# Performance work log

Hardware: AMD Instinct MI355X
Metric: run time of the kernel (lower is better)

## Reference

```python
import jax, jax.numpy as jnp
import numpy as np
from math import factorial, sqrt

L_OUT = 4      # max_degree / max_actp_degree -> 25 sph components
L_B = 2        # max_basis_degree -> 9 sph components
F = 16         # num_radial_features (feature channels)
N_ATOMS = 10000
N_BONDS = 80000
CUTOFF = 5.0

# ---------------- real Clebsch-Gordan coefficients (numpy, at import) ----------

def _cg(j1, m1, j2, m2, j3, m3):
    if m1 + m2 != m3 or not (abs(j1 - j2) <= j3 <= j1 + j2):
        return 0.0
    f = factorial
    pre = sqrt((2 * j3 + 1) * f(j1 + j2 - j3) * f(j1 - j2 + j3) * f(-j1 + j2 + j3) / f(j1 + j2 + j3 + 1))
    pre *= sqrt(f(j1 + m1) * f(j1 - m1) * f(j2 + m2) * f(j2 - m2) * f(j3 + m3) * f(j3 - m3))
    s = 0.0
    kmin = max(0, j2 - j3 - m1, j1 - j3 + m2)
    kmax = min(j1 + j2 - j3, j1 - m1, j2 + m2)
    for k in range(kmin, kmax + 1):
        s += (-1) ** k / (f(k) * f(j1 + j2 - j3 - k) * f(j1 - m1 - k) * f(j2 + m2 - k) * f(j3 - j2 + m1 + k) * f(j3 - j1 - m2 + k))
    return pre * s

def _U(l):
    # complex->real spherical harmonic change of basis (Condon-Shortley)
    U = np.zeros((2 * l + 1, 2 * l + 1), dtype=complex)
    U[l, l] = 1.0
    for m in range(1, l + 1):
        U[l + m, l + m] = (-1) ** m / np.sqrt(2.0)
        U[l + m, l - m] = 1.0 / np.sqrt(2.0)
        U[l - m, l + m] = -1j * (-1) ** m / np.sqrt(2.0)
        U[l - m, l - m] = 1j / np.sqrt(2.0)
    return U

def _real_cg(l1, l2, l3):
    Cc = np.zeros((2 * l1 + 1, 2 * l2 + 1, 2 * l3 + 1), dtype=complex)
    for m1 in range(-l1, l1 + 1):
        for m2 in range(-l2, l2 + 1):
            m3 = m1 + m2
            if -l3 <= m3 <= l3:
                Cc[l1 + m1, l2 + m2, l3 + m3] = _cg(l1, m1, l2, m2, l3, m3)
    Cr = np.einsum('am,bn,ck,mnk->abc', _U(l1).conj(), _U(l2).conj(), _U(l3), Cc)
    out = Cr.real + Cr.imag  # exactly one of the two is nonzero per path
    out[np.abs(out) < 1e-12] = 0.0
    return out

PATHS = []
for _l1 in range(L_B + 1):
    for _l2 in range(L_OUT + 1):
        for _l3 in range(abs(_l1 - _l2), min(_l1 + _l2, L_OUT) + 1):
            PATHS.append((_l1, _l2, _l3, jnp.asarray(_real_cg(_l1, _l2, _l3), dtype=jnp.float32)))
N_PATHS = len(PATHS)

# ---------------- equivariant building blocks --------------------------------

def _sph(u):
    # real spherical harmonics l=0..2, m=-l..l, for unit vectors u (E,3)
    x, y, z = u[:, 0], u[:, 1], u[:, 2]
    c0 = 0.28209479177387814
    c1 = 0.4886025119029199
    c2a = 1.0925484305920792
    c2b = 0.31539156525252005
    c2c = 0.5462742152960396
    return jnp.stack([jnp.full_like(x, c0),
                      c1 * y, c1 * z, c1 * x,
                      c2a * x * y, c2a * y * z, c2b * (3 * z * z - 1.0), c2a * x * z, c2c * (x * x - y * y)],
                     axis=-1)  # (E,9)

def basis(disp):
    r = jnp.linalg.norm(disp, axis=-1)
    u = disp / (r[:, None] + 1e-12)
    Y = _sph(u)  # (E,9)
    centers = jnp.linspace(0.0, CUTOFF, F)
    width = CUTOFF / F
    rb = jnp.exp(-((r[:, None] - centers) / width) ** 2)  # (E,F)
    cut = jnp.where(r < CUTOFF, 0.5 * (jnp.cos(jnp.pi * r / CUTOFF) + 1.0), 0.0)
    rb = rb * cut[:, None]
    return Y[:, None, :, None] * rb[:, None, None, :]

def edense(x, W, b):
    # per-(parity,degree) feature mixing; bias only on even scalar channel
    nl = W.shape[1]
    outs = []
    for l in range(nl):
        lo, hi = l * l, (l + 1) * (l + 1)
        outs.append(jnp.einsum('epmf,pfg->epmg', x[:, :, lo:hi], W[:, l]))
    out = jnp.concatenate(outs, axis=2)
    return out.at[:, 0, 0, :].add(b)

def eln(x, gamma, beta, eps=1e-5):
    # equivariant LayerNorm: RMS of per-feature degree norms; standard LN on even scalar
    outs = []
    for l in range(L_OUT + 1):
        lo, hi = l * l, (l + 1) * (l + 1)
        blk = x[:, :, lo:hi]
        n2 = jnp.sum(blk * blk, axis=2)                       # (E,2,F)
        rms = jnp.sqrt(jnp.mean(n2, axis=-1, keepdims=True) + eps)  # (E,2,1)
        outs.append(blk / rms[..., None] * gamma[:, l][None, :, None, :])
    out = jnp.concatenate(outs, axis=2)
    s = x[:, 0, 0, :]
    mu = jnp.mean(s, axis=-1, keepdims=True)
    var = jnp.var(s, axis=-1, keepdims=True)
    sh = (s - mu) / jnp.sqrt(var + eps) * gamma[0, 0] + beta
    return out.at[:, 0, 0, :].set(sh)

def emish(x):
    s = x[:, 0, 0, :]
    sp = jax.nn.softplus(s)
    t = jnp.tanh(sp)
    f = s * t
    fp = t + s * (1.0 - t * t) * jax.nn.sigmoid(s)
    out = x * fp[:, None, None, :]
    return out.at[:, 0, 0, :].set(f)

def tensor_product(x1, x2, Wtp):
    # FusedTensor analogue: x1 (E,1,9,F) parity (-1)^l per degree; x2 (E,2,25,F)
    x1s = x1[:, 0]
    out = jnp.zeros_like(x2)
    for i, (l1, l2, l3, C) in enumerate(PATHS):
        a = x1s[:, l1 * l1:(l1 + 1) * (l1 + 1)]          # (E,n1,F)
        b = x2[:, :, l2 * l2:(l2 + 1) * (l2 + 1)]        # (E,2,n2,F)
        tmp = jnp.einsum('enf,epmf,nmk->epkf', a, b, C)  # (E,2,n3,F)
        tmp = tmp * Wtp[i][None, :, None, :]
        if l1 % 2 == 1:
            tmp = tmp[:, ::-1]  # odd l1 flips output parity
        out = out.at[:, :, l3 * l3:(l3 + 1) * (l3 + 1)].add(tmp)
    return out

def forward(atomic_descriptors, neighbour_indices, neighbour_displacements,
            W1, b1, gamma, beta, W2, b2, Wb, bb, Wtp):
    i, j = neighbour_indices[:, 0], neighbour_indices[:, 1]
    y = atomic_descriptors[i] + atomic_descriptors[j]  # (E,2,25,F)
    y = edense(y, W1, b1)
    y = eln(y, gamma, beta)
    y = emish(y)
    y = edense(y, W2, b2) + y
    be = basis(neighbour_displacements).astype(jnp.float32)  # (E,1,9,F)
    bed = edense(be, Wb, bb)
    return tensor_product(bed, y, Wtp)

# ---------------- harness ----------------------------------------------------

def setup_inputs() -> dict:
    key = jax.random.key(0)
    ks = jax.random.split(key, 8)
    scale = 1.0 / np.sqrt(F)
    return {
        'atomic_descriptors': jax.random.normal(ks[0], (N_ATOMS, 2, (L_OUT + 1) ** 2, F), jnp.float32),
        'neighbour_indices': jax.random.randint(ks[1], (N_BONDS, 2), 0, N_ATOMS),
        'neighbour_displacements': jax.random.normal(ks[2], (N_BONDS, 3), jnp.float32),
        'W1': jax.random.normal(ks[3], (2, L_OUT + 1, F, F), jnp.float32) * scale,
        'b1': jnp.zeros((F,), jnp.float32),
        'gamma': jnp.ones((2, L_OUT + 1, F), jnp.float32),
        'beta': jnp.zeros((F,), jnp.float32),
        'W2': jax.random.normal(ks[4], (2, L_OUT + 1, F, F), jnp.float32) * scale,
        'b2': jnp.zeros((F,), jnp.float32),
        'Wb': jax.random.normal(ks[5], (1, L_B + 1, F, F), jnp.float32) * scale,
        'bb': jnp.zeros((F,), jnp.float32),
        'Wtp': jax.random.normal(ks[6], (N_PATHS, 2, F), jnp.float32) * scale,
    }

def reference(atomic_descriptors, neighbour_indices, neighbour_displacements,
              W1, b1, gamma, beta, W2, b2, Wb, bb, Wtp):
    return forward(atomic_descriptors, neighbour_indices, neighbour_displacements,
                   W1, b1, gamma, beta, W2, b2, Wb, bb, Wtp)
```

## Files before the change

### kernel.cpp

```cpp
#include <hip/hip_runtime.h>
#include <hip/hip_fp16.h>

#define NF   16
#define NLM  25
#define BPB  16
#define YSTR 816

typedef _Float16 h2f __attribute__((ext_vector_type(2)));

#if defined(__has_builtin)
#if __has_builtin(__builtin_amdgcn_fdot2)
#define FDOT2(a,b,c) __builtin_amdgcn_fdot2((a),(b),(c),false)
#endif
#endif
#ifndef FDOT2
#define FDOT2(a,b,c) ((c) + (float)(a)[0]*(float)(b)[0] + (float)(a)[1]*(float)(b)[1])
#endif

#define WAVE_LDS_FENCE() asm volatile("" ::: "memory")

#define NT_STORE(p, v) __builtin_nontemporal_store((v), (p))

constexpr double FT[12] = {1.,1.,2.,6.,24.,120.,720.,5040.,40320.,362880.,3628800.,39916800.};

constexpr double csqrt(double x){
    if (x <= 0.0) return 0.0;
    double g = x > 1.0 ? x : 1.0;
    for (int i = 0; i < 60; ++i){ double n = 0.5*(g + x/g); if (n == g) break; g = n; }
    return g;
}

constexpr double cgc(int j1,int m1,int j2,int m2,int j3,int m3){
    if (m1 + m2 != m3) return 0.0;
    int dj = j1 > j2 ? j1 - j2 : j2 - j1;
    if (j3 < dj || j3 > j1 + j2) return 0.0;
    if (m1 < -j1 || m1 > j1 || m2 < -j2 || m2 > j2 || m3 < -j3 || m3 > j3) return 0.0;
    double X = (2*j3+1)*FT[j1+j2-j3]*FT[j1-j2+j3]*FT[-j1+j2+j3]/FT[j1+j2+j3+1];
    double Y = FT[j1+m1]*FT[j1-m1]*FT[j2+m2]*FT[j2-m2]*FT[j3+m3]*FT[j3-m3];
    double pre = csqrt(X*Y);
    double s = 0.0;
    int kmin = 0; if (j2-j3-m1 > kmin) kmin = j2-j3-m1; if (j1-j3+m2 > kmin) kmin = j1-j3+m2;
    int kmax = j1+j2-j3; if (j1-m1 < kmax) kmax = j1-m1; if (j2+m2 < kmax) kmax = j2+m2;
    for (int k = kmin; k <= kmax; ++k)
        s += ((k & 1) ? -1.0 : 1.0) /
             (FT[k]*FT[j1+j2-j3-k]*FT[j1-m1-k]*FT[j2+m2-k]*FT[j3-j2+m1+k]*FT[j3-j1-m2+k]);
    return pre*s;
}

struct cplx { double re, im; };

constexpr cplx Uent(int l, int a, int col){
    int mp = a - l, mm = col - l;
    const double s2 = 0.70710678118654752440;
    if (mp == 0) return (mm == 0) ? cplx{1.0,0.0} : cplx{0.0,0.0};
    if (mp > 0){
        double sgn = (mp & 1) ? -1.0 : 1.0;
        if (mm ==  mp) return cplx{sgn*s2, 0.0};
        if (mm == -mp) return cplx{s2, 0.0};
        return cplx{0.0,0.0};
    }
    int q = -mp; double sgn = (q & 1) ? -1.0 : 1.0;
    if (mm ==  q) return cplx{0.0, -sgn*s2};
    if (mm == -q) return cplx{0.0,  s2};
    return cplx{0.0,0.0};
}

constexpr double realcg(int l1,int l2,int l3,int a,int b,int c){
    double re = 0.0, im = 0.0;
    for (int m = -l1; m <= l1; ++m){
        cplx u1 = Uent(l1, a, l1+m); u1.im = -u1.im;
        if (u1.re == 0.0 && u1.im == 0.0) continue;
        for (int n = -l2; n <= l2; ++n){
            cplx u2 = Uent(l2, b, l2+n); u2.im = -u2.im;
            if (u2.re == 0.0 && u2.im == 0.0) continue;
            int k = m + n; if (k < -l3 || k > l3) continue;
            cplx u3 = Uent(l3, c, l3+k);
            if (u3.re == 0.0 && u3.im == 0.0) continue;
            double g = cgc(l1, m, l2, n, l3, k);
            if (g == 0.0) continue;
            double pr = u1.re*u2.re - u1.im*u2.im;
            double pi = u1.re*u2.im + u1.im*u2.re;
            re += (pr*u3.re - pi*u3.im)*g;
            im += (pr*u3.im + pi*u3.re)*g;
        }
    }
    double o = re + im;
    if (o < 1e-12 && o > -1e-12) o = 0.0;
    return o;
}

template<int L1,int L2,int L3> struct CGT { float v[2*L1+1][2*L2+1][2*L3+1]; };

template<int L1,int L2,int L3>
constexpr CGT<L1,L2,L3> makeCG(){
    CGT<L1,L2,L3> t{};
    for (int a = 0; a < 2*L1+1; ++a)
        for (int b = 0; b < 2*L2+1; ++b)
            for (int c = 0; c < 2*L3+1; ++c)
                t.v[a][b][c] = (float)realcg(L1, L2, L3, a, b, c);
    return t;
}

template<int L1,int L2,int L3,int PIDX>
__device__ __forceinline__ void tp_path(const float (&bed)[9], const float (&y)[2][NLM],
                                        float (&o)[2][NLM], const float* __restrict__ Wtp, int g){
    static constexpr CGT<L1,L2,L3> C = makeCG<L1,L2,L3>();
    constexpr int K = 2*L3+1;
    float a0[K], a1[K];
    #pragma unroll
    for (int k = 0; k < K; ++k){ a0[k] = 0.f; a1[k] = 0.f; }
    #pragma unroll
    for (int n = 0; n < 2*L1+1; ++n){
        const float bn = bed[L1*L1 + n];
        #pragma unroll
        for (int m = 0; m < 2*L2+1; ++m){
            const float p0 = bn * y[0][L2*L2 + m];
            const float p1 = bn * y[1][L2*L2 + m];
            #pragma unroll
            for (int k = 0; k < K; ++k){
                const float c = C.v[n][m][k];
                if (c != 0.f){
                    a0[k] = fmaf(c, p0, a0[k]);
                    a1[k] = fmaf(c, p1, a1[k]);
                }
            }
        }
    }
    const float w0 = Wtp[(PIDX*2 + 0)*NF + g];
    const float w1 = Wtp[(PIDX*2 + 1)*NF + g];
    #pragma unroll
    for (int k = 0; k < K; ++k){
        if (L1 & 1){
            o[0][L3*L3 + k] = fmaf(w1, a1[k], o[0][L3*L3 + k]);
            o[1][L3*L3 + k] = fmaf(w0, a0[k], o[1][L3*L3 + k]);
        } else {
            o[0][L3*L3 + k] = fmaf(w0, a0[k], o[0][L3*L3 + k]);
            o[1][L3*L3 + k] = fmaf(w1, a1[k], o[1][L3*L3 + k]);
        }
    }
}

__global__ void transpose_w(const float* __restrict__ W1, const float* __restrict__ W2,
                            const float* __restrict__ Wb, void* __restrict__ wsv){
    __half* h1 = (__half*)wsv;
    __half* h2 = h1 + 2560;
    float*  wb = (float*)(h1 + 5120);
    int idx = blockIdx.x*256 + threadIdx.x;
    if (idx < 2560){
        int mat = idx >> 8, r = (idx >> 4) & 15, c = idx & 15;
        h1[idx] = __float2half_rn(W1[mat*256 + c*16 + r]);
        h2[idx] = __float2half_rn(W2[mat*256 + c*16 + r]);
    } else if (idx < 3328){
        int k = idx - 2560; int mat = k >> 8, r = (k >> 4) & 15, c = k & 15;
        wb[k] = Wb[mat*256 + c*16 + r];
    }
}

struct H8 { float4 a, b; };

__global__ __launch_bounds__(256, 3)
void bctmd_kernel(const float* __restrict__ A, const int* __restrict__ nbr,
                  const float* __restrict__ disp,
                  const float* __restrict__ b1, const float* __restrict__ gamma,
                  const float* __restrict__ beta, const float* __restrict__ b2,
                  const float* __restrict__ bb, const float* __restrict__ Wtp,
                  const __half* __restrict__ Wt1h, const __half* __restrict__ Wt2h,
                  const float* __restrict__ Wtb,
                  float* __restrict__ out, int nb)
{
    __shared__ __align__(16) __half ybuf[BPB*YSTR];
    const int tid  = threadIdx.x;
    const int bl   = tid >> 4;
    const int g    = tid & 15;
    const int bond = blockIdx.x*BPB + bl;
    const bool act = bond < nb;
    __half* yb = &ybuf[bl*YSTR];

    if (act){
        const int i = nbr[2*bond], j = nbr[2*bond+1];
        const float4* Ai = (const float4*)(A + (size_t)i*800);
        const float4* Aj = (const float4*)(A + (size_t)j*800);
        #pragma unroll
        for (int it = 0; it < 13; ++it){
            int q = g + 16*it;
            if (q < 200){
                float4 a = Ai[q], b = Aj[q];
                __half2* d = (__half2*)&yb[4*q];
                d[0] = __float22half2_rn(make_float2(a.x+b.x, a.y+b.y));
                d[1] = __float22half2_rn(make_float2(a.z+b.z, a.w+b.w));
            }
        }
    }
    WAVE_LDS_FENCE();

    float y[2][NLM];
    if (act){
        #pragma unroll
        for (int p = 0; p < 2; ++p){
            #pragma unroll
            for (int l = 0; l < 5; ++l){
                H8 wv = *(const H8*)(Wt1h + (((p*5 + l)*16 + g) << 4));
                const h2f* w = (const h2f*)&wv;
                #pragma unroll
                for (int m = 0; m < 2*l+1; ++m){
                    const int lm = l*l + m;
                    H8 rv = *(const H8*)&yb[p*400 + lm*16];
                    const h2f* v = (const h2f*)&rv;
                    float acc = 0.f;
                    #pragma unroll
                    for (int q = 0; q < 8; ++q) acc = FDOT2(v[q], w[q], acc);
                    y[p][lm] = acc;
                }
            }
        }
        y[0][0] += b1[g];

        float s0 = y[0][0];
        #pragma unroll
        for (int p = 0; p < 2; ++p){
            #pragma unroll
            for (int l = 0; l < 5; ++l){
                float n2 = 0.f;
                #pragma unroll
                for (int m = 0; m < 2*l+1; ++m){ float v = y[p][l*l+m]; n2 = fmaf(v, v, n2); }
                #pragma unroll
                for (int d = 1; d < 16; d <<= 1) n2 += __shfl_xor(n2, d, 16);
                float rinv = rsqrtf(n2*(1.f/16.f) + 1e-5f);
                float sc = rinv * gamma[(p*5 + l)*16 + g];
                #pragma unroll
                for (int m = 0; m < 2*l+1; ++m) y[p][l*l+m] *= sc;
            }
        }
        float mu = s0, sq = s0*s0;
        #pragma unroll
        for (int d = 1; d < 16; d <<= 1){ mu += __shfl_xor(mu, d, 16); sq += __shfl_xor(sq, d, 16); }
        mu *= (1.f/16.f); sq *= (1.f/16.f);
        float var = sq - mu*mu;
        float sh = (s0 - mu)*rsqrtf(var + 1e-5f)*gamma[g] + beta[g];
        y[0][0] = sh;

        float s  = sh;
        float es = __expf(fminf(s, 30.f));
        float es2 = es*es;
        float t   = (es2 + 2.f*es) / (es2 + 2.f*es + 2.f);
        float sig = es / (1.f + es);
        float fv  = s*t;
        float fp  = t + s*(1.f - t*t)*sig;
        #pragma unroll
        for (int p = 0; p < 2; ++p)
            #pragma unroll
            for (int lm = 0; lm < NLM; ++lm) y[p][lm] *= fp;
        y[0][0] = fv;
    }
    WAVE_LDS_FENCE();

    if (act){
        #pragma unroll
        for (int p = 0; p < 2; ++p)
            #pragma unroll
            for (int lm = 0; lm < NLM; ++lm)
                yb[p*400 + lm*16 + g] = __float2half_rn(y[p][lm]);
    }
    WAVE_LDS_FENCE();

    if (act){
        #pragma unroll
        for (int p = 0; p < 2; ++p){
            #pragma unroll
            for (int l = 0; l < 5; ++l){
                H8 wv = *(const H8*)(Wt2h + (((p*5 + l)*16 + g) << 4));
                const h2f* w = (const h2f*)&wv;
                #pragma unroll
                for (int m = 0; m < 2*l+1; ++m){
                    const int lm = l*l + m;
                    H8 rv = *(const H8*)&yb[p*400 + lm*16];
                    const h2f* v = (const h2f*)&rv;
                    float acc = 0.f;
                    #pragma unroll
                    for (int q = 0; q < 8; ++q) acc = FDOT2(v[q], w[q], acc);
                    y[p][lm] += acc;
                }
            }
        }
        y[0][0] += b2[g];

        float dx = disp[3*bond], dy = disp[3*bond+1], dz = disp[3*bond+2];
        float r  = sqrtf(dx*dx + dy*dy + dz*dz);
        float ir = 1.f/(r + 1e-12f);
        float ux = dx*ir, uy = dy*ir, uz = dz*ir;
        float Y[9];
        Y[0] = 0.28209479177387814f;
        Y[1] = 0.4886025119029199f*uy; Y[2] = 0.4886025119029199f*uz; Y[3] = 0.4886025119029199f*ux;
        Y[4] = 1.0925484305920792f*ux*uy; Y[5] = 1.0925484305920792f*uy*uz;
        Y[6] = 0.31539156525252005f*(3.f*uz*uz - 1.f);
        Y[7] = 1.0925484305920792f*ux*uz; Y[8] = 0.5462742152960396f*(ux*ux - uy*uy);
        float cut = (r < 5.0f) ? 0.5f*(__cosf(r*0.62831853071795864769f) + 1.f) : 0.f;
        float rb[16];
        #pragma unroll
        for (int f = 0; f < 16; ++f){
            float d = (r - (float)f*(1.f/3.f))*3.2f;
            rb[f] = __expf(-d*d)*cut;
        }
        float t3[3];
        #pragma unroll
        for (int l = 0; l < 3; ++l){
            const float4* wp = (const float4*)(Wtb + (l*16 + g)*16);
            float acc = 0.f;
            #pragma unroll
            for (int q = 0; q < 4; ++q){
                float4 t = wp[q];
                acc = fmaf(rb[4*q],   t.x, acc);
                acc = fmaf(rb[4*q+1], t.y, acc);
                acc = fmaf(rb[4*q+2], t.z, acc);
                acc = fmaf(rb[4*q+3], t.w, acc);
            }
            t3[l] = acc;
        }
        float bed[9];
        bed[0] = Y[0]*t3[0] + bb[g];
        #pragma unroll
        for (int m = 1; m < 4; ++m) bed[m] = Y[m]*t3[1];
        #pragma unroll
        for (int m = 4; m < 9; ++m) bed[m] = Y[m]*t3[2];

        float o[2][NLM];
        #pragma unroll
        for (int p = 0; p < 2; ++p)
            #pragma unroll
            for (int lm = 0; lm < NLM; ++lm) o[p][lm] = 0.f;

        tp_path<0,0,0, 0>(bed, y, o, Wtp, g);
        tp_path<0,1,1, 1>(bed, y, o, Wtp, g);
        tp_path<0,2,2, 2>(bed, y, o, Wtp, g);
        tp_path<0,3,3, 3>(bed, y, o, Wtp, g);
        tp_path<0,4,4, 4>(bed, y, o, Wtp, g);
        tp_path<1,0,1, 5>(bed, y, o, Wtp, g);
        tp_path<1,1,0, 6>(bed, y, o, Wtp, g);
        tp_path<1,1,1, 7>(bed, y, o, Wtp, g);
        tp_path<1,1,2, 8>(bed, y, o, Wtp, g);
        tp_path<1,2,1, 9>(bed, y, o, Wtp, g);
        tp_path<1,2,2,10>(bed, y, o, Wtp, g);
        tp_path<1,2,3,11>(bed, y, o, Wtp, g);
        tp_path<1,3,2,12>(bed, y, o, Wtp, g);
        tp_path<1,3,3,13>(bed, y, o, Wtp, g);
        tp_path<1,3,4,14>(bed, y, o, Wtp, g);
        tp_path<1,4,3,15>(bed, y, o, Wtp, g);
        tp_path<1,4,4,16>(bed, y, o, Wtp, g);
        tp_path<2,0,2,17>(bed, y, o, Wtp, g);
        tp_path<2,1,1,18>(bed, y, o, Wtp, g);
        tp_path<2,1,2,19>(bed, y, o, Wtp, g);
        tp_path<2,1,3,20>(bed, y, o, Wtp, g);
        tp_path<2,2,0,21>(bed, y, o, Wtp, g);
        tp_path<2,2,1,22>(bed, y, o, Wtp, g);
        tp_path<2,2,2,23>(bed, y, o, Wtp, g);
        tp_path<2,2,3,24>(bed, y, o, Wtp, g);
        tp_path<2,2,4,25>(bed, y, o, Wtp, g);
        tp_path<2,3,1,26>(bed, y, o, Wtp, g);
        tp_path<2,3,2,27>(bed, y, o, Wtp, g);
        tp_path<2,3,3,28>(bed, y, o, Wtp, g);
        tp_path<2,3,4,29>(bed, y, o, Wtp, g);
        tp_path<2,4,2,30>(bed, y, o, Wtp, g);
        tp_path<2,4,3,31>(bed, y, o, Wtp, g);
        tp_path<2,4,4,32>(bed, y, o, Wtp, g);

        float* op = out + (size_t)bond*800;
        #pragma unroll
        for (int p = 0; p < 2; ++p)
            #pragma unroll
            for (int lm = 0; lm < NLM; ++lm)
                NT_STORE(&op[p*400 + lm*16 + g], o[p][lm]);
    }
}

extern "C" void kernel_launch(void* const* d_in, const int* in_sizes, int n_in,
                              void* d_out, int out_size, void* d_ws, size_t ws_size,
                              hipStream_t stream){
    const float* A     = (const float*)d_in[0];
    const int*   nbr   = (const int*)d_in[1];
    const float* disp  = (const float*)d_in[2];
    const float* W1    = (const float*)d_in[3];
    const float* b1    = (const float*)d_in[4];
    const float* gamma = (const float*)d_in[5];
    const float* beta  = (const float*)d_in[6];
    const float* W2    = (const float*)d_in[7];
    const float* b2    = (const float*)d_in[8];
    const float* Wb    = (const float*)d_in[9];
    const float* bb    = (const float*)d_in[10];
    const float* Wtp   = (const float*)d_in[11];

    const int nb = in_sizes[1] / 2;

    hipLaunchKernelGGL(transpose_w, dim3(13), dim3(256), 0, stream, W1, W2, Wb, d_ws);

    const __half* h1 = (const __half*)d_ws;
    const __half* h2 = h1 + 2560;
    const float*  wb = (const float*)(h1 + 5120);

    const int nblk = (nb + BPB - 1) / BPB;
    hipLaunchKernelGGL(bctmd_kernel, dim3(nblk), dim3(256), 0, stream,
                       A, nbr, disp, b1, gamma, beta, b2, bb, Wtp,
                       h1, h2, wb, (float*)d_out, nb);
}
```

Before: 185.9 us.

## Split fused bond kernel into MLP and tensor-product kernels via workspace

Splits the single fused kernel into two launches: one runs the gather plus two-layer equivariant MLP and writes the fp16 intermediate per bond to workspace, and the other reads it back and runs the spherical-harmonic tensor product. The aim is to lower per-kernel register pressure and raise occupancy, since the first kernel asks for four blocks per CU. In exchange it adds an extra global round trip of about 128 MB of fp16 intermediate plus a second launch, and it adds one more fp16 rounding of y before the tensor product. If the workspace is too small it falls back to the fused kernel.

```diff
diff --git a/kernel.cpp b/kernel.cpp
--- a/kernel.cpp
+++ b/kernel.cpp
@@ -18,7 +18,6 @@
 #endif
 
 #define WAVE_LDS_FENCE() asm volatile("" ::: "memory")
-
 #define NT_STORE(p, v) __builtin_nontemporal_store((v), (p))
 
 constexpr double FT[12] = {1.,1.,2.,6.,24.,120.,720.,5040.,40320.,362880.,3628800.,39916800.};
@@ -158,6 +157,261 @@
 
 struct H8 { float4 a, b; };
 
+__device__ __forceinline__ void mlp_body(const float* __restrict__ A, const int* __restrict__ nbr,
+                                         const float* __restrict__ b1, const float* __restrict__ gamma,
+                                         const float* __restrict__ beta, const float* __restrict__ b2,
+                                         const __half* __restrict__ Wt1h, const __half* __restrict__ Wt2h,
+                                         __half* yb, int bond, int g, bool act, float (&y)[2][NLM]){
+    if (act){
+        const int i = nbr[2*bond], j = nbr[2*bond+1];
+        const float4* Ai = (const float4*)(A + (size_t)i*800);
+        const float4* Aj = (const float4*)(A + (size_t)j*800);
+        #pragma unroll
+        for (int it = 0; it < 13; ++it){
+            int q = g + 16*it;
+            if (q < 200){
+                float4 a = Ai[q], b = Aj[q];
+                __half2* d = (__half2*)&yb[4*q];
+                d[0] = __float22half2_rn(make_float2(a.x+b.x, a.y+b.y));
+                d[1] = __float22half2_rn(make_float2(a.z+b.z, a.w+b.w));
+            }
+        }
+    }
+    WAVE_LDS_FENCE();
+
+    if (act){
+        #pragma unroll
+        for (int p = 0; p < 2; ++p){
+            #pragma unroll
+            for (int l = 0; l < 5; ++l){
+                H8 wv = *(const H8*)(Wt1h + (((p*5 + l)*16 + g) << 4));
+                const h2f* w = (const h2f*)&wv;
+                #pragma unroll
+                for (int m = 0; m < 2*l+1; ++m){
+                    const int lm = l*l + m;
+                    H8 rv = *(const H8*)&yb[p*400 + lm*16];
+                    const h2f* v = (const h2f*)&rv;
+                    float acc = 0.f;
+                    #pragma unroll
+                    for (int q = 0; q < 8; ++q) acc = FDOT2(v[q], w[q], acc);
+                    y[p][lm] = acc;
+                }
+            }
+        }
+        y[0][0] += b1[g];
+
+        float s0 = y[0][0];
+        #pragma unroll
+        for (int p = 0; p < 2; ++p){
+            #pragma unroll
+            for (int l = 0; l < 5; ++l){
+                float n2 = 0.f;
+                #pragma unroll
+                for (int m = 0; m < 2*l+1; ++m){ float v = y[p][l*l+m]; n2 = fmaf(v, v, n2); }
+                #pragma unroll
+                for (int d = 1; d < 16; d <<= 1) n2 += __shfl_xor(n2, d, 16);
+                float rinv = rsqrtf(n2*(1.f/16.f) + 1e-5f);
+                float sc = rinv * gamma[(p*5 + l)*16 + g];
+                #pragma unroll
+                for (int m = 0; m < 2*l+1; ++m) y[p][l*l+m] *= sc;
+            }
+        }
+        float mu = s0, sq = s0*s0;
+        #pragma unroll
+        for (int d = 1; d < 16; d <<= 1){ mu += __shfl_xor(mu, d, 16); sq += __shfl_xor(sq, d, 16); }
+        mu *= (1.f/16.f); sq *= (1.f/16.f);
+        float var = sq - mu*mu;
+        float sh = (s0 - mu)*rsqrtf(var + 1e-5f)*gamma[g] + beta[g];
+        y[0][0] = sh;
+
+        float s  = sh;
+        float es = __expf(fminf(s, 30.f));
+        float es2 = es*es;
+        float t   = (es2 + 2.f*es) / (es2 + 2.f*es + 2.f);
+        float sig = es / (1.f + es);
+        float fv  = s*t;
+        float fp  = t + s*(1.f - t*t)*sig;
+        #pragma unroll
+        for (int p = 0; p < 2; ++p)
+            #pragma unroll
+            for (int lm = 0; lm < NLM; ++lm) y[p][lm] *= fp;
+        y[0][0] = fv;
+    }
+    WAVE_LDS_FENCE();
+
+    if (act){
+        #pragma unroll
+        for (int p = 0; p < 2; ++p)
+            #pragma unroll
+            for (int lm = 0; lm < NLM; ++lm)
+                yb[p*400 + lm*16 + g] = __float2half_rn(y[p][lm]);
+    }
+    WAVE_LDS_FENCE();
+
+    if (act){
+        #pragma unroll
+        for (int p = 0; p < 2; ++p){
+            #pragma unroll
+            for (int l = 0; l < 5; ++l){
+                H8 wv = *(const H8*)(Wt2h + (((p*5 + l)*16 + g) << 4));
+                const h2f* w = (const h2f*)&wv;
+                #pragma unroll
+                for (int m = 0; m < 2*l+1; ++m){
+                    const int lm = l*l + m;
+                    H8 rv = *(const H8*)&yb[p*400 + lm*16];
+                    const h2f* v = (const h2f*)&rv;
+                    float acc = 0.f;
+                    #pragma unroll
+                    for (int q = 0; q < 8; ++q) acc = FDOT2(v[q], w[q], acc);
+                    y[p][lm] += acc;
+                }
+            }
+        }
+        y[0][0] += b2[g];
+    }
+}
+
+__device__ __forceinline__ void tp_body(const float* __restrict__ disp, const float* __restrict__ bb,
+                                        const float* __restrict__ Wtp, const float* __restrict__ Wtb,
+                                        float* __restrict__ out, int bond, int g,
+                                        const float (&y)[2][NLM]){
+    float dx = disp[3*bond], dy = disp[3*bond+1], dz = disp[3*bond+2];
+    float r  = sqrtf(dx*dx + dy*dy + dz*dz);
+    float ir = 1.f/(r + 1e-12f);
+    float ux = dx*ir, uy = dy*ir, uz = dz*ir;
+    float Y[9];
+    Y[0] = 0.28209479177387814f;
+    Y[1] = 0.4886025119029199f*uy; Y[2] = 0.4886025119029199f*uz; Y[3] = 0.4886025119029199f*ux;
+    Y[4] = 1.0925484305920792f*ux*uy; Y[5] = 1.0925484305920792f*uy*uz;
+    Y[6] = 0.31539156525252005f*(3.f*uz*uz - 1.f);
+    Y[7] = 1.0925484305920792f*ux*uz; Y[8] = 0.5462742152960396f*(ux*ux - uy*uy);
+    float cut = (r < 5.0f) ? 0.5f*(__cosf(r*0.62831853071795864769f) + 1.f) : 0.f;
+    float rb[16];
+    #pragma unroll
+    for (int f = 0; f < 16; ++f){
+        float d = (r - (float)f*(1.f/3.f))*3.2f;
+        rb[f] = __expf(-d*d)*cut;
+    }
+    float t3[3];
+    #pragma unroll
+    for (int l = 0; l < 3; ++l){
+        const float4* wp = (const float4*)(Wtb + (l*16 + g)*16);
+        float acc = 0.f;
+        #pragma unroll
+        for (int q = 0; q < 4; ++q){
+            float4 t = wp[q];
+            acc = fmaf(rb[4*q],   t.x, acc);
+            acc = fmaf(rb[4*q+1], t.y, acc);
+            acc = fmaf(rb[4*q+2], t.z, acc);
+            acc = fmaf(rb[4*q+3], t.w, acc);
+        }
+        t3[l] = acc;
+    }
+    float bed[9];
+    bed[0] = Y[0]*t3[0] + bb[g];
+    #pragma unroll
+    for (int m = 1; m < 4; ++m) bed[m] = Y[m]*t3[1];
+    #pragma unroll
+    for (int m = 4; m < 9; ++m) bed[m] = Y[m]*t3[2];
+
+    float o[2][NLM];
+    #pragma unroll
+    for (int p = 0; p < 2; ++p)
+        #pragma unroll
+        for (int lm = 0; lm < NLM; ++lm) o[p][lm] = 0.f;
+
+    tp_path<0,0,0, 0>(bed, y, o, Wtp, g);
+    tp_path<0,1,1, 1>(bed, y, o, Wtp, g);
+    tp_path<0,2,2, 2>(bed, y, o, Wtp, g);
+    tp_path<0,3,3, 3>(bed, y, o, Wtp, g);
+    tp_path<0,4,4, 4>(bed, y, o, Wtp, g);
+    tp_path<1,0,1, 5>(bed, y, o, Wtp, g);
+    tp_path<1,1,0, 6>(bed, y, o, Wtp, g);
+    tp_path<1,1,1, 7>(bed, y, o, Wtp, g);
+    tp_path<1,1,2, 8>(bed, y, o, Wtp, g);
+    tp_path<1,2,1, 9>(bed, y, o, Wtp, g);
+    tp_path<1,2,2,10>(bed, y, o, Wtp, g);
+    tp_path<1,2,3,11>(bed, y, o, Wtp, g);
+    tp_path<1,3,2,12>(bed, y, o, Wtp, g);
+    tp_path<1,3,3,13>(bed, y, o, Wtp, g);
+    tp_path<1,3,4,14>(bed, y, o, Wtp, g);
+    tp_path<1,4,3,15>(bed, y, o, Wtp, g);
+    tp_path<1,4,4,16>(bed, y, o, Wtp, g);
+    tp_path<2,0,2,17>(bed, y, o, Wtp, g);
+    tp_path<2,1,1,18>(bed, y, o, Wtp, g);
+    tp_path<2,1,2,19>(bed, y, o, Wtp, g);
+    tp_path<2,1,3,20>(bed, y, o, Wtp, g);
+    tp_path<2,2,0,21>(bed, y, o, Wtp, g);
+    tp_path<2,2,1,22>(bed, y, o, Wtp, g);
+    tp_path<2,2,2,23>(bed, y, o, Wtp, g);
+    tp_path<2,2,3,24>(bed, y, o, Wtp, g);
+    tp_path<2,2,4,25>(bed, y, o, Wtp, g);
+    tp_path<2,3,1,26>(bed, y, o, Wtp, g);
+    tp_path<2,3,2,27>(bed, y, o, Wtp, g);
+    tp_path<2,3,3,28>(bed, y, o, Wtp, g);
+    tp_path<2,3,4,29>(bed, y, o, Wtp, g);
+    tp_path<2,4,2,30>(bed, y, o, Wtp, g);
+    tp_path<2,4,3,31>(bed, y, o, Wtp, g);
+    tp_path<2,4,4,32>(bed, y, o, Wtp, g);
+
+    float* op = out + (size_t)bond*800;
+    #pragma unroll
+    for (int p = 0; p < 2; ++p)
+        #pragma unroll
+        for (int lm = 0; lm < NLM; ++lm)
+            NT_STORE(&op[p*400 + lm*16 + g], o[p][lm]);
+}
+
+__global__ __launch_bounds__(256, 4)
+void bctmd_front(const float* __restrict__ A, const int* __restrict__ nbr,
+                 const float* __restrict__ b1, const float* __restrict__ gamma,
+                 const float* __restrict__ beta, const float* __restrict__ b2,
+                 const __half* __restrict__ Wt1h, const __half* __restrict__ Wt2h,
+                 __half* __restrict__ yws, int nb)
+{
+    __shared__ __align__(16) __half ybuf[BPB*YSTR];
+    const int tid  = threadIdx.x;
+    const int bl   = tid >> 4;
+    const int g    = tid & 15;
+    const int bond = blockIdx.x*BPB + bl;
+    const bool act = bond < nb;
+    __half* yb = &ybuf[bl*YSTR];
+
+    float y[2][NLM];
+    mlp_body(A, nbr, b1, gamma, beta, b2, Wt1h, Wt2h, yb, bond, g, act, y);
+
+    if (act){
+        __half* yo = yws + (size_t)bond*800;
+        #pragma unroll
+        for (int p = 0; p < 2; ++p)
+            #pragma unroll
+            for (int lm = 0; lm < NLM; ++lm)
+                yo[p*400 + lm*16 + g] = __float2half_rn(y[p][lm]);
+    }
+}
+
+__global__ __launch_bounds__(256, 3)
+void bctmd_tp(const __half* __restrict__ yws, const float* __restrict__ disp,
+              const float* __restrict__ bb, const float* __restrict__ Wtp,
+              const float* __restrict__ Wtb, float* __restrict__ out, int nb)
+{
+    const int tid  = threadIdx.x;
+    const int bl   = tid >> 4;
+    const int g    = tid & 15;
+    const int bond = blockIdx.x*BPB + bl;
+    if (bond >= nb) return;
+
+    float y[2][NLM];
+    const __half* yi = yws + (size_t)bond*800;
+    #pragma unroll
+    for (int p = 0; p < 2; ++p)
+        #pragma unroll
+        for (int lm = 0; lm < NLM; ++lm)
+            y[p][lm] = __half2float(yi[p*400 + lm*16 + g]);
+
+    tp_body(disp, bb, Wtp, Wtb, out, bond, g, y);
+}
+
 __global__ __launch_bounds__(256, 3)
 void bctmd_kernel(const float* __restrict__ A, const int* __restrict__ nbr,
                   const float* __restrict__ disp,
@@ -176,200 +430,10 @@
     const bool act = bond < nb;
     __half* yb = &ybuf[bl*YSTR];
 
-    if (act){
-        const int i = nbr[2*bond], j = nbr[2*bond+1];
-        const float4* Ai = (const float4*)(A + (size_t)i*800);
-        const float4* Aj = (const float4*)(A + (size_t)j*800);
-        #pragma unroll
-        for (int it = 0; it < 13; ++it){
-            int q = g + 16*it;
-            if (q < 200){
-                float4 a = Ai[q], b = Aj[q];
-                __half2* d = (__half2*)&yb[4*q];
-                d[0] = __float22half2_rn(make_float2(a.x+b.x, a.y+b.y));
-                d[1] = __float22half2_rn(make_float2(a.z+b.z, a.w+b.w));
-            }
-        }
-    }
-    WAVE_LDS_FENCE();
-
     float y[2][NLM];
-    if (act){
-        #pragma unroll
-        for (int p = 0; p < 2; ++p){
-            #pragma unroll
-            for (int l = 0; l < 5; ++l){
-                H8 wv = *(const H8*)(Wt1h + (((p*5 + l)*16 + g) << 4));
-                const h2f* w = (const h2f*)&wv;
-                #pragma unroll
-                for (int m = 0; m < 2*l+1; ++m){
-                    const int lm = l*l + m;
-                    H8 rv = *(const H8*)&yb[p*400 + lm*16];
-                    const h2f* v = (const h2f*)&rv;
-                    float acc = 0.f;
-                    #pragma unroll
-                    for (int q = 0; q < 8; ++q) acc = FDOT2(v[q], w[q], acc);
-                    y[p][lm] = acc;
-                }
-            }
-        }
-        y[0][0] += b1[g];
-
-        float s0 = y[0][0];
-        #pragma unroll
-        for (int p = 0; p < 2; ++p){
-            #pragma unroll
-            for (int l = 0; l < 5; ++l){
-                float n2 = 0.f;
-                #pragma unroll
-                for (int m = 0; m < 2*l+1; ++m){ float v = y[p][l*l+m]; n2 = fmaf(v, v, n2); }
-                #pragma unroll
-                for (int d = 1; d < 16; d <<= 1) n2 += __shfl_xor(n2, d, 16);
-                float rinv = rsqrtf(n2*(1.f/16.f) + 1e-5f);
-                float sc = rinv * gamma[(p*5 + l)*16 + g];
-                #pragma unroll
-                for (int m = 0; m < 2*l+1; ++m) y[p][l*l+m] *= sc;
-            }
-        }
-        float mu = s0, sq = s0*s0;
-        #pragma unroll
-        for (int d = 1; d < 16; d <<= 1){ mu += __shfl_xor(mu, d, 16); sq += __shfl_xor(sq, d, 16); }
-        mu *= (1.f/16.f); sq *= (1.f/16.f);
-        float var = sq - mu*mu;
-        float sh = (s0 - mu)*rsqrtf(var + 1e-5f)*gamma[g] + beta[g];
-        y[0][0] = sh;
-
-        float s  = sh;
-        float es = __expf(fminf(s, 30.f));
-        float es2 = es*es;
-        float t   = (es2 + 2.f*es) / (es2 + 2.f*es + 2.f);
-        float sig = es / (1.f + es);
-        float fv  = s*t;
-        float fp  = t + s*(1.f - t*t)*sig;
-        #pragma unroll
-        for (int p = 0; p < 2; ++p)
-            #pragma unroll
-            for (int lm = 0; lm < NLM; ++lm) y[p][lm] *= fp;
-        y[0][0] = fv;
-    }
-    WAVE_LDS_FENCE();
-
-    if (act){
-        #pragma unroll
-        for (int p = 0; p < 2; ++p)
-            #pragma unroll
-            for (int lm = 0; lm < NLM; ++lm)
-                yb[p*400 + lm*16 + g] = __float2half_rn(y[p][lm]);
-    }
-    WAVE_LDS_FENCE();
-
-    if (act){
-        #pragma unroll
-        for (int p = 0; p < 2; ++p){
-            #pragma unroll
-            for (int l = 0; l < 5; ++l){
-                H8 wv = *(const H8*)(Wt2h + (((p*5 + l)*16 + g) << 4));
-                const h2f* w = (const h2f*)&wv;
-                #pragma unroll
-                for (int m = 0; m < 2*l+1; ++m){
-                    const int lm = l*l + m;
-                    H8 rv = *(const H8*)&yb[p*400 + lm*16];
-                    const h2f* v = (const h2f*)&rv;
-                    float acc = 0.f;
-                    #pragma unroll
-                    for (int q = 0; q < 8; ++q) acc = FDOT2(v[q], w[q], acc);
-                    y[p][lm] += acc;
-                }
-            }
-        }
-        y[0][0] += b2[g];
-
-        float dx = disp[3*bond], dy = disp[3*bond+1], dz = disp[3*bond+2];
-        float r  = sqrtf(dx*dx + dy*dy + dz*dz);
-        float ir = 1.f/(r + 1e-12f);
-        float ux = dx*ir, uy = dy*ir, uz = dz*ir;
-        float Y[9];
-        Y[0] = 0.28209479177387814f;
-        Y[1] = 0.4886025119029199f*uy; Y[2] = 0.4886025119029199f*uz; Y[3] = 0.4886025119029199f*ux;
-        Y[4] = 1.0925484305920792f*ux*uy; Y[5] = 1.0925484305920792f*uy*uz;
-        Y[6] = 0.31539156525252005f*(3.f*uz*uz - 1.f);
-        Y[7] = 1.0925484305920792f*ux*uz; Y[8] = 0.5462742152960396f*(ux*ux - uy*uy);
-        float cut = (r < 5.0f) ? 0.5f*(__cosf(r*0.62831853071795864769f) + 1.f) : 0.f;
-        float rb[16];
-        #pragma unroll
-        for (int f = 0; f < 16; ++f){
-            float d = (r - (float)f*(1.f/3.f))*3.2f;
-            rb[f] = __expf(-d*d)*cut;
-        }
-        float t3[3];
-        #pragma unroll
-        for (int l = 0; l < 3; ++l){
-            const float4* wp = (const float4*)(Wtb + (l*16 + g)*16);
-            float acc = 0.f;
-            #pragma unroll
-            for (int q = 0; q < 4; ++q){
-                float4 t = wp[q];
-                acc = fmaf(rb[4*q],   t.x, acc);
-                acc = fmaf(rb[4*q+1], t.y, acc);
-                acc = fmaf(rb[4*q+2], t.z, acc);
-                acc = fmaf(rb[4*q+3], t.w, acc);
-            }
-            t3[l] = acc;
-        }
-        float bed[9];
-        bed[0] = Y[0]*t3[0] + bb[g];
-        #pragma unroll
-        for (int m = 1; m < 4; ++m) bed[m] = Y[m]*t3[1];
-        #pragma unroll
-        for (int m = 4; m < 9; ++m) bed[m] = Y[m]*t3[2];
-
-        float o[2][NLM];
-        #pragma unroll
-        for (int p = 0; p < 2; ++p)
-            #pragma unroll
-            for (int lm = 0; lm < NLM; ++lm) o[p][lm] = 0.f;
-
-        tp_path<0,0,0, 0>(bed, y, o, Wtp, g);
-        tp_path<0,1,1, 1>(bed, y, o, Wtp, g);
-        tp_path<0,2,2, 2>(bed, y, o, Wtp, g);
-        tp_path<0,3,3, 3>(bed, y, o, Wtp, g);
-        tp_path<0,4,4, 4>(bed, y, o, Wtp, g);
-        tp_path<1,0,1, 5>(bed, y, o, Wtp, g);
-        tp_path<1,1,0, 6>(bed, y, o, Wtp, g);
-        tp_path<1,1,1, 7>(bed, y, o, Wtp, g);
-        tp_path<1,1,2, 8>(bed, y, o, Wtp, g);
-        tp_path<1,2,1, 9>(bed, y, o, Wtp, g);
-        tp_path<1,2,2,10>(bed, y, o, Wtp, g);
-        tp_path<1,2,3,11>(bed, y, o, Wtp, g);
-        tp_path<1,3,2,12>(bed, y, o, Wtp, g);
-        tp_path<1,3,3,13>(bed, y, o, Wtp, g);
-        tp_path<1,3,4,14>(bed, y, o, Wtp, g);
-        tp_path<1,4,3,15>(bed, y, o, Wtp, g);
-        tp_path<1,4,4,16>(bed, y, o, Wtp, g);
-        tp_path<2,0,2,17>(bed, y, o, Wtp, g);
-        tp_path<2,1,1,18>(bed, y, o, Wtp, g);
-        tp_path<2,1,2,19>(bed, y, o, Wtp, g);
-        tp_path<2,1,3,20>(bed, y, o, Wtp, g);
-        tp_path<2,2,0,21>(bed, y, o, Wtp, g);
-        tp_path<2,2,1,22>(bed, y, o, Wtp, g);
-        tp_path<2,2,2,23>(bed, y, o, Wtp, g);
-        tp_path<2,2,3,24>(bed, y, o, Wtp, g);
-        tp_path<2,2,4,25>(bed, y, o, Wtp, g);
-        tp_path<2,3,1,26>(bed, y, o, Wtp, g);
-        tp_path<2,3,2,27>(bed, y, o, Wtp, g);
-        tp_path<2,3,3,28>(bed, y, o, Wtp, g);
-        tp_path<2,3,4,29>(bed, y, o, Wtp, g);
-        tp_path<2,4,2,30>(bed, y, o, Wtp, g);
-        tp_path<2,4,3,31>(bed, y, o, Wtp, g);
-        tp_path<2,4,4,32>(bed, y, o, Wtp, g);
-
-        float* op = out + (size_t)bond*800;
-        #pragma unroll
-        for (int p = 0; p < 2; ++p)
-            #pragma unroll
-            for (int lm = 0; lm < NLM; ++lm)
-                NT_STORE(&op[p*400 + lm*16 + g], o[p][lm]);
-    }
+    mlp_body(A, nbr, b1, gamma, beta, b2, Wt1h, Wt2h, yb, bond, g, act, y);
+
+    if (act) tp_body(disp, bb, Wtp, Wtb, out, bond, g, y);
 }
 
 extern "C" void kernel_launch(void* const* d_in, const int* in_sizes, int n_in,
@@ -397,7 +461,18 @@
     const float*  wb = (const float*)(h1 + 5120);
 
     const int nblk = (nb + BPB - 1) / BPB;
-    hipLaunchKernelGGL(bctmd_kernel, dim3(nblk), dim3(256), 0, stream,
-                       A, nbr, disp, b1, gamma, beta, b2, bb, Wtp,
-                       h1, h2, wb, (float*)d_out, nb);
-}
+    const size_t y_off   = 16384;
+    const size_t y_bytes = (size_t)nb * 800 * sizeof(__half);
+
+    if (ws_size >= y_off + y_bytes){
+        __half* yws = (__half*)((char*)d_ws + y_off);
+        hipLaunchKernelGGL(bctmd_front, dim3(nblk), dim3(256), 0, stream,
+                           A, nbr, b1, gamma, beta, b2, h1, h2, yws, nb);
+        hipLaunchKernelGGL(bctmd_tp, dim3(nblk), dim3(256), 0, stream,
+                           yws, disp, bb, Wtp, wb, (float*)d_out, nb);
+    } else {
+        hipLaunchKernelGGL(bctmd_kernel, dim3(nblk), dim3(256), 0, stream,
+                           A, nbr, disp, b1, gamma, beta, b2, bb, Wtp,
+                           h1, h2, wb, (float*)d_out, nb);
+    }
+}
```

Measured after the change: 198.8 us. +7.0%, slower.
